# Performance work log

Measured on AMD Instinct MI355X. Metric: run time of the kernel, lower is better.

## Reference

```python
import jax, jax.numpy as jnp
import numpy as np

B, T, E = 1024, 200, 64
NU, NM, NC = 100000, 1000000, 1000
D_LAU_IN = 8 * E      # 512
D_MLP_IN = 7 * E      # 448
EPS = 1e-5
NEG = -2.0 ** 31


def setup_inputs() -> dict:
    key = jax.random.key(0)
    ks = jax.random.split(key, 32)
    f = lambda k, shape, s=0.05: (jax.random.normal(k, shape, dtype=jnp.float32) * s)
    inp = {
        "uid": jax.random.randint(ks[0], (B,), 0, NU, dtype=jnp.int32),
        "mid": jax.random.randint(ks[1], (B,), 0, NM, dtype=jnp.int32),
        "cat": jax.random.randint(ks[2], (B,), 0, NC, dtype=jnp.int32),
        "historical_mid": jax.random.randint(ks[3], (B, T), 0, NM, dtype=jnp.int32),
        "historical_cat": jax.random.randint(ks[4], (B, T), 0, NC, dtype=jnp.int32),
        "mask": jax.random.randint(ks[5], (B, T), 0, 2, dtype=jnp.int32),
        # embedding tables
        "user_table": f(ks[6], (NU, E), 0.1),
        "mat_table": f(ks[7], (NM, E), 0.1),
        "cat_table": f(ks[8], (NC, E), 0.1),
        # LocalActivationUnit: Linear(512,256)->Sigmoid->Linear(256,128)->Sigmoid->Linear(128,1)
        "lau_w1": f(ks[9], (D_LAU_IN, 256)), "lau_b1": f(ks[10], (256,)),
        "lau_w2": f(ks[11], (256, 128)),     "lau_b2": f(ks[12], (128,)),
        "lau_w3": f(ks[13], (128, 1)),       "lau_b3": f(ks[14], (1,)),
        # MLP: BN(448)->Linear(448,512)->BN->LeakyReLU(0.1)->Linear(512,256)->BN->LeakyReLU->Linear(256,2)
        "bn0_g": jnp.ones((D_MLP_IN,), jnp.float32), "bn0_b": jnp.zeros((D_MLP_IN,), jnp.float32),
        "mlp_w1": f(ks[15], (D_MLP_IN, 512)), "mlp_b1": f(ks[16], (512,)),
        "bn1_g": jnp.ones((512,), jnp.float32), "bn1_b": jnp.zeros((512,), jnp.float32),
        "mlp_w2": f(ks[17], (512, 256)),      "mlp_b2": f(ks[18], (256,)),
        "bn2_g": jnp.ones((256,), jnp.float32), "bn2_b": jnp.zeros((256,), jnp.float32),
        "mlp_w3": f(ks[19], (256, 2)),        "mlp_b3": f(ks[20], (2,)),
    }
    return inp


def _bn(x, g, b):
    # torch BatchNorm1d in training mode: batch mean, biased variance
    mu = jnp.mean(x, axis=0)
    var = jnp.var(x, axis=0)
    return (x - mu) * jax.lax.rsqrt(var + EPS) * g + b


def reference(uid, mid, cat, historical_mid, historical_cat, mask,
              user_table, mat_table, cat_table,
              lau_w1, lau_b1, lau_w2, lau_b2, lau_w3, lau_b3,
              bn0_g, bn0_b, mlp_w1, mlp_b1, bn1_g, bn1_b,
              mlp_w2, mlp_b2, bn2_g, bn2_b, mlp_w3, mlp_b3):
    u = user_table[uid]                                             # [B,E]
    cur = jnp.concatenate([mat_table[mid], cat_table[cat]], axis=1)  # [B,2E]
    hist = jnp.concatenate([mat_table[historical_mid],
                            cat_table[historical_cat]], axis=2)      # [B,T,2E]
    maskf = mask.astype(hist.dtype)                                  # [B,T]

    # Local activation unit
    cur_e = jnp.broadcast_to(cur[:, None, :], hist.shape)            # [B,T,2E]
    comb = jnp.concatenate([cur_e, hist, cur_e - hist, cur_e * hist], axis=2)  # [B,T,8E]
    h = jax.nn.sigmoid(comb @ lau_w1 + lau_b1)
    h = jax.nn.sigmoid(h @ lau_w2 + lau_b2)
    aw = (h @ lau_w3 + lau_b3)[..., 0]                               # [B,T]
    masked = jnp.where(mask == 1, aw, jnp.asarray(NEG, aw.dtype))
    scores = jax.nn.softmax(masked, axis=-1) * maskf                 # [B,T]
    lau = jnp.einsum('bt,bte->be', scores, hist)                     # [B,2E]

    # masked mean of history
    hsum = jnp.einsum('bt,bte->be', maskf, hist)
    hmean = hsum / jnp.sum(maskf, axis=1, keepdims=True)

    x = jnp.concatenate([u, cur, lau, hmean], axis=-1)               # [B,7E]
    x = _bn(x, bn0_g, bn0_b)
    x = jax.nn.leaky_relu(_bn(x @ mlp_w1 + mlp_b1, bn1_g, bn1_b), 0.1)
    x = jax.nn.leaky_relu(_bn(x @ mlp_w2 + mlp_b2, bn2_g, bn2_b), 0.1)
    return x @ mlp_w3 + mlp_b3                                        # [B,2]
```

## Files before the change

### kernel.cpp

```cpp
#include <hip/hip_runtime.h>

#define BB 1024
#define TT 200
#define MROWS (BB*TT)

typedef unsigned short u16;
typedef __attribute__((ext_vector_type(8))) short bf16x8;
typedef __attribute__((ext_vector_type(4))) float f32x4;

__device__ __forceinline__ u16 f2bf(float f) {
  unsigned u = __float_as_uint(f);
  u += 0x7fff + ((u >> 16) & 1);
  return (u16)(u >> 16);
}
__device__ __forceinline__ float bf2f(u16 h) {
  return __uint_as_float(((unsigned)h) << 16);
}

__global__ void prep_weights(const float* __restrict__ w1, const float* __restrict__ w2,
                             u16* __restrict__ WpT, float* __restrict__ Wq,
                             u16* __restrict__ W2T) {
  int i = blockIdx.x * 256 + threadIdx.x;
  if (i < 65536) {
    int n = i >> 8, k = i & 255;
    float v;
    if (k < 128) v = w1[(128 + k) * 256 + n] - w1[(256 + k) * 256 + n];
    else         v = w1[(384 + (k - 128)) * 256 + n];
    WpT[n * 256 + k] = f2bf(v);
  } else if (i < 98304) {
    int j = i - 65536;
    int k = j >> 8, jc = j & 255;
    Wq[j] = w1[k * 256 + jc] + w1[(256 + k) * 256 + jc];
  } else if (i < 131072) {
    int j = i - 98304;
    int n = j >> 8, k = j & 255;
    W2T[j] = f2bf(w2[k * 128 + n]);
  }
}

__global__ __launch_bounds__(256) void prep_batch(
    const int* __restrict__ mid, const int* __restrict__ cat,
    const float* __restrict__ mat_table, const float* __restrict__ cat_table,
    const float* __restrict__ lau_b1, const float* __restrict__ Wq,
    float* __restrict__ cur, float* __restrict__ bias1p) {
  int b = blockIdx.x, tid = threadIdx.x;
  __shared__ float curL[128];
  if (tid < 64)        curL[tid] = mat_table[(long)mid[b] * 64 + tid];
  else if (tid < 128)  curL[tid] = cat_table[(long)cat[b] * 64 + (tid - 64)];
  __syncthreads();
  if (tid < 128) cur[b * 128 + tid] = curL[tid];
  float s = lau_b1[tid];
  for (int k = 0; k < 128; ++k) s += curL[k] * Wq[k * 256 + tid];
  bias1p[b * 256 + tid] = s;
}

__global__ __launch_bounds__(256) void lau_fused(
    const int* __restrict__ hmid, const int* __restrict__ hcat,
    const float* __restrict__ mat_table, const float* __restrict__ cat_table,
    const float* __restrict__ cur, const float* __restrict__ bias1p,
    const u16* __restrict__ WpT, const u16* __restrict__ W2T,
    const float* __restrict__ b2, const float* __restrict__ w3,
    const float* __restrict__ b3,
    u16* __restrict__ Xh, float* __restrict__ AW) {
  __shared__ __align__(16) u16 Al[64 * 264];
  __shared__ float awp[4][64];
  int tid = threadIdx.x, wave = tid >> 6, l = tid & 63;
  int q = l >> 4, r16 = l & 15;
  long mBase = (long)blockIdx.x * 64;

  for (int i = tid; i < 2048; i += 256) {
    int r = i >> 5, c4 = i & 31;
    long bt = mBase + r;
    int b = (int)(bt / TT);
    int e0 = c4 * 4;
    float4 hv;
    if (e0 < 64) hv = *(const float4*)(mat_table + (long)hmid[bt] * 64 + e0);
    else         hv = *(const float4*)(cat_table + (long)hcat[bt] * 64 + (e0 - 64));
    float4 cv = *(const float4*)(cur + b * 128 + e0);
    u16 hb[4] = {f2bf(hv.x), f2bf(hv.y), f2bf(hv.z), f2bf(hv.w)};
    u16 pb[4] = {f2bf(hv.x * cv.x), f2bf(hv.y * cv.y), f2bf(hv.z * cv.z), f2bf(hv.w * cv.w)};
    *(ushort4*)(Al + r * 264 + e0)       = *(ushort4*)hb;
    *(ushort4*)(Al + r * 264 + 128 + e0) = *(ushort4*)pb;
    *(ushort4*)(Xh + bt * 128 + e0)      = *(ushort4*)hb;
  }
  __syncthreads();

  f32x4 acc1[4][4] = {};
  const u16* wp1 = WpT + ((long)(wave * 64 + r16)) * 256 + q * 8;
  #pragma unroll
  for (int ki = 0; ki < 8; ++ki) {
    bf16x8 a[4];
    #pragma unroll
    for (int mt = 0; mt < 4; ++mt)
      a[mt] = *(const bf16x8*)(Al + (mt * 16 + r16) * 264 + ki * 32 + q * 8);
    #pragma unroll
    for (int nt = 0; nt < 4; ++nt) {
      bf16x8 bq = *(const bf16x8*)(wp1 + nt * (16 * 256) + ki * 32);
      #pragma unroll
      for (int mt = 0; mt < 4; ++mt)
        acc1[mt][nt] = __builtin_amdgcn_mfma_f32_16x16x32_bf16(a[mt], bq, acc1[mt][nt], 0, 0, 0);
    }
  }
  __syncthreads();
  #pragma unroll
  for (int mt = 0; mt < 4; ++mt)
    #pragma unroll
    for (int r = 0; r < 4; ++r) {
      int row = mt * 16 + q * 4 + r;
      int bidx = (int)((mBase + row) / TT);
      const float* bp = bias1p + (long)bidx * 256;
      #pragma unroll
      for (int nt = 0; nt < 4; ++nt) {
        int col = wave * 64 + nt * 16 + r16;
        float z = acc1[mt][nt][r] + bp[col];
        Al[row * 264 + col] = f2bf(1.f / (1.f + __expf(-z)));
      }
    }
  __syncthreads();

  f32x4 acc2[4][2] = {};
  const u16* wp2 = W2T + ((long)(wave * 32 + r16)) * 256 + q * 8;
  #pragma unroll
  for (int ki = 0; ki < 8; ++ki) {
    bf16x8 a[4];
    #pragma unroll
    for (int mt = 0; mt < 4; ++mt)
      a[mt] = *(const bf16x8*)(Al + (mt * 16 + r16) * 264 + ki * 32 + q * 8);
    #pragma unroll
    for (int nt = 0; nt < 2; ++nt) {
      bf16x8 bq = *(const bf16x8*)(wp2 + nt * (16 * 256) + ki * 32);
      #pragma unroll
      for (int mt = 0; mt < 4; ++mt)
        acc2[mt][nt] = __builtin_amdgcn_mfma_f32_16x16x32_bf16(a[mt], bq, acc2[mt][nt], 0, 0, 0);
    }
  }
  float rp[4][4];
  #pragma unroll
  for (int mt = 0; mt < 4; ++mt)
    #pragma unroll
    for (int r = 0; r < 4; ++r) rp[mt][r] = 0.f;
  #pragma unroll
  for (int nt = 0; nt < 2; ++nt) {
    int col = wave * 32 + nt * 16 + r16;
    float b2v = b2[col], w3v = w3[col];
    #pragma unroll
    for (int mt = 0; mt < 4; ++mt)
      #pragma unroll
      for (int r = 0; r < 4; ++r) {
        float z = acc2[mt][nt][r] + b2v;
        rp[mt][r] += w3v / (1.f + __expf(-z));
      }
  }
  #pragma unroll
  for (int off = 1; off < 16; off <<= 1)
    #pragma unroll
    for (int mt = 0; mt < 4; ++mt)
      #pragma unroll
      for (int r = 0; r < 4; ++r)
        rp[mt][r] += __shfl_xor(rp[mt][r], off, 16);
  if (r16 == 0)
    #pragma unroll
    for (int mt = 0; mt < 4; ++mt)
      #pragma unroll
      for (int r = 0; r < 4; ++r)
        awp[wave][mt * 16 + q * 4 + r] = rp[mt][r];
  __syncthreads();
  if (tid < 64)
    AW[mBase + tid] = awp[0][tid] + awp[1][tid] + awp[2][tid] + awp[3][tid] + b3[0];
}

__global__ __launch_bounds__(256) void softmax_pool(
    const float* __restrict__ AW, const int* __restrict__ mask,
    const int* __restrict__ uid, const float* __restrict__ user_table,
    const float* __restrict__ cur, const u16* __restrict__ Xh,
    float* __restrict__ Xmlp) {
  int b = blockIdx.x, tid = threadIdx.x;
  __shared__ float red[256];
  __shared__ float sc[TT], mkf[TT];
  __shared__ float ps[512];
  int mk = 0;
  float masked = -3.0e38f;
  if (tid < TT) {
    mk = mask[b * TT + tid];
    masked = mk ? AW[b * TT + tid] : -2147483648.0f;
  }
  red[tid] = masked; __syncthreads();
  for (int s = 128; s > 0; s >>= 1) { if (tid < s) red[tid] = fmaxf(red[tid], red[tid + s]); __syncthreads(); }
  float mx = red[0]; __syncthreads();
  float ev = (tid < TT) ? __expf(masked - mx) : 0.f;
  red[tid] = ev; __syncthreads();
  for (int s = 128; s > 0; s >>= 1) { if (tid < s) red[tid] += red[tid + s]; __syncthreads(); }
  float denom = red[0]; __syncthreads();
  red[tid] = (tid < TT) ? (float)mk : 0.f; __syncthreads();
  for (int s = 128; s > 0; s >>= 1) { if (tid < s) red[tid] += red[tid + s]; __syncthreads(); }
  float cnt = red[0]; __syncthreads();
  if (tid < TT) { sc[tid] = (ev / denom) * (float)mk; mkf[tid] = (float)mk; }
  __syncthreads();
  int c = tid & 127, p = tid >> 7;
  const u16* xb = Xh + (long)b * TT * 128 + c;
  float sL = 0.f, sH = 0.f;
  for (int t = p; t < TT; t += 2) {
    float hv = bf2f(xb[(long)t * 128]);
    sL += sc[t] * hv;
    sH += mkf[t] * hv;
  }
  ps[tid] = sL; ps[256 + tid] = sH;
  __syncthreads();
  if (tid < 128) {
    float lau  = ps[tid] + ps[tid + 128];
    float hsum = ps[256 + tid] + ps[256 + tid + 128];
    Xmlp[b * 448 + 192 + tid] = lau;
    Xmlp[b * 448 + 320 + tid] = hsum / cnt;
  } else {
    int j = tid - 128;
    Xmlp[b * 448 + 64 + j] = cur[b * 128 + j];
    if (j < 64) Xmlp[b * 448 + j] = user_table[(long)uid[b] * 64 + j];
  }
}

__global__ __launch_bounds__(256) void colstats(const float* __restrict__ X, int cols,
                                                float* __restrict__ psum,
                                                float* __restrict__ psq) {
  int cg = blockIdx.x, rc = blockIdx.y;
  int c = threadIdx.x & 63, ty = threadIdx.x >> 6;
  int col = cg * 64 + c;
  float s = 0.f, ss = 0.f;
  for (int i = 0; i < 16; ++i) {
    int r = rc * 64 + ty + i * 4;
    float v = X[(long)r * cols + col];
    s += v; ss += v * v;
  }
  __shared__ float s1[256], s2[256];
  s1[threadIdx.x] = s; s2[threadIdx.x] = ss;
  __syncthreads();
  if (ty == 0) {
    s  = s1[c] + s1[c + 64] + s1[c + 128] + s1[c + 192];
    ss = s2[c] + s2[c + 64] + s2[c + 128] + s2[c + 192];
    psum[rc * cols + col] = s;
    psq [rc * cols + col] = ss;
  }
}

template <bool LEAKY>
__global__ __launch_bounds__(256) void gemm_bn(
    const float* __restrict__ A, int K,
    const float* __restrict__ psumA, const float* __restrict__ psqA,
    const float* __restrict__ g, const float* __restrict__ bta,
    const float* __restrict__ W, const float* __restrict__ bias, int N,
    float* __restrict__ C, float* __restrict__ psumC, float* __restrict__ psqC) {
  __shared__ float As[16][65], Bs[16][65];
  __shared__ float scK[512], shK[512];
  __shared__ float colS[16][64], colQ[16][64];
  int tid = threadIdx.x;
  for (int j = tid; j < K; j += 256) {
    float s = 0.f, ss = 0.f;
    for (int rc = 0; rc < 16; ++rc) { s += psumA[rc * K + j]; ss += psqA[rc * K + j]; }
    float mu = s * (1.f / 1024.f), var = ss * (1.f / 1024.f) - mu * mu;
    float scv = rsqrtf(var + 1e-5f) * g[j];
    scK[j] = scv; shK[j] = bta[j] - mu * scv;
  }
  __syncthreads();
  int m0 = blockIdx.x * 64, n0 = blockIdx.y * 64;
  int tx = tid & 15, ty = tid >> 4;
  float acc[4][4] = {};
  for (int k0 = 0; k0 < K; k0 += 16) {
    __syncthreads();
    for (int i = tid; i < 1024; i += 256) {
      int m = i >> 4, k = i & 15;
      float v = A[(long)(m0 + m) * K + k0 + k] * scK[k0 + k] + shK[k0 + k];
      if (LEAKY) v = v > 0.f ? v : 0.1f * v;
      As[k][m] = v;
    }
    for (int i = tid; i < 1024; i += 256) {
      int k = i >> 6, n = i & 63;
      Bs[k][n] = W[(long)(k0 + k) * N + n0 + n];
    }
    __syncthreads();
    for (int k = 0; k < 16; ++k) {
      float a[4], bq[4];
      for (int ii = 0; ii < 4; ++ii) a[ii]  = As[k][ty * 4 + ii];
      for (int jj = 0; jj < 4; ++jj) bq[jj] = Bs[k][tx * 4 + jj];
      for (int ii = 0; ii < 4; ++ii)
        for (int jj = 0; jj < 4; ++jj) acc[ii][jj] += a[ii] * bq[jj];
    }
  }
  float cs4[4], cq4[4];
  for (int jj = 0; jj < 4; ++jj) {
    int n = n0 + tx * 4 + jj;
    float bv = bias[n];
    float cs = 0.f, cq = 0.f;
    for (int ii = 0; ii < 4; ++ii) {
      float val = acc[ii][jj] + bv;
      C[(long)(m0 + ty * 4 + ii) * N + n] = val;
      cs += val; cq += val * val;
    }
    cs4[jj] = cs; cq4[jj] = cq;
  }
  __syncthreads();
  for (int jj = 0; jj < 4; ++jj) {
    colS[ty][tx * 4 + jj] = cs4[jj];
    colQ[ty][tx * 4 + jj] = cq4[jj];
  }
  __syncthreads();
  if (tid < 64) {
    float s = 0.f, ss = 0.f;
    for (int t = 0; t < 16; ++t) { s += colS[t][tid]; ss += colQ[t][tid]; }
    psumC[blockIdx.x * N + n0 + tid] = s;
    psqC [blockIdx.x * N + n0 + tid] = ss;
  }
}

__global__ __launch_bounds__(256) void final_out(
    const float* __restrict__ y2,
    const float* __restrict__ psum2, const float* __restrict__ psq2,
    const float* __restrict__ g, const float* __restrict__ bta,
    const float* __restrict__ w3, const float* __restrict__ b3,
    float* __restrict__ out) {
  __shared__ float sc2[256], sh2[256];
  __shared__ float p0[256], p1[256];
  int tid = threadIdx.x;
  {
    float s = 0.f, ss = 0.f;
    for (int rc = 0; rc < 16; ++rc) { s += psum2[rc * 256 + tid]; ss += psq2[rc * 256 + tid]; }
    float mu = s * (1.f / 1024.f), var = ss * (1.f / 1024.f) - mu * mu;
    float scv = rsqrtf(var + 1e-5f) * g[tid];
    sc2[tid] = scv; sh2[tid] = bta[tid] - mu * scv;
  }
  __syncthreads();
  int row = blockIdx.x * 64 + (tid >> 2), q = tid & 3;
  const float* yr = y2 + (long)row * 256;
  float a0 = 0.f, a1 = 0.f;
  for (int k = q * 64; k < q * 64 + 64; ++k) {
    float v = yr[k] * sc2[k] + sh2[k];
    v = v > 0.f ? v : 0.1f * v;
    a0 += v * w3[2 * k];
    a1 += v * w3[2 * k + 1];
  }
  p0[tid] = a0; p1[tid] = a1;
  __syncthreads();
  if (q == 0) {
    out[row * 2 + 0] = p0[tid] + p0[tid + 1] + p0[tid + 2] + p0[tid + 3] + b3[0];
    out[row * 2 + 1] = p1[tid] + p1[tid + 1] + p1[tid + 2] + p1[tid + 3] + b3[1];
  }
}


extern "C" void kernel_launch(void* const* d_in, const int* in_sizes, int n_in,
                              void* d_out, int out_size, void* d_ws, size_t ws_size,
                              hipStream_t stream) {
  const int* uid  = (const int*)d_in[0];
  const int* mid  = (const int*)d_in[1];
  const int* cat  = (const int*)d_in[2];
  const int* hmid = (const int*)d_in[3];
  const int* hcat = (const int*)d_in[4];
  const int* mask = (const int*)d_in[5];
  const float* user_table = (const float*)d_in[6];
  const float* mat_table  = (const float*)d_in[7];
  const float* cat_table  = (const float*)d_in[8];
  const float* lau_w1 = (const float*)d_in[9];
  const float* lau_b1 = (const float*)d_in[10];
  const float* lau_w2 = (const float*)d_in[11];
  const float* lau_b2 = (const float*)d_in[12];
  const float* lau_w3 = (const float*)d_in[13];
  const float* lau_b3 = (const float*)d_in[14];
  const float* bn0_g = (const float*)d_in[15];
  const float* bn0_b = (const float*)d_in[16];
  const float* mlp_w1 = (const float*)d_in[17];
  const float* mlp_b1 = (const float*)d_in[18];
  const float* bn1_g = (const float*)d_in[19];
  const float* bn1_b = (const float*)d_in[20];
  const float* mlp_w2 = (const float*)d_in[21];
  const float* mlp_b2 = (const float*)d_in[22];
  const float* bn2_g = (const float*)d_in[23];
  const float* bn2_b = (const float*)d_in[24];
  const float* mlp_w3 = (const float*)d_in[25];
  const float* mlp_b3 = (const float*)d_in[26];
  float* out = (float*)d_out;

  char* w = (char*)d_ws;
  size_t off = 0;
  auto take = [&](size_t bytes) { size_t o = off; off += (bytes + 255) & ~(size_t)255; return o; };
  u16*   Xh     = (u16*)  (w + take((size_t)MROWS * 128 * 2));
  float* AW     = (float*)(w + take((size_t)MROWS * 4));
  float* cur    = (float*)(w + take((size_t)BB * 128 * 4));
  float* bias1p = (float*)(w + take((size_t)BB * 256 * 4));
  float* xmlp   = (float*)(w + take((size_t)BB * 448 * 4));
  float* y1     = (float*)(w + take((size_t)BB * 512 * 4));
  float* y2     = (float*)(w + take((size_t)BB * 256 * 4));
  u16*   WpT    = (u16*)  (w + take(256 * 256 * 2));
  float* Wq     = (float*)(w + take(128 * 256 * 4));
  u16*   W2T    = (u16*)  (w + take(128 * 256 * 2));
  float* psum0  = (float*)(w + take(16 * 448 * 4));
  float* psq0   = (float*)(w + take(16 * 448 * 4));
  float* psum1  = (float*)(w + take(16 * 512 * 4));
  float* psq1   = (float*)(w + take(16 * 512 * 4));
  float* psum2  = (float*)(w + take(16 * 256 * 4));
  float* psq2   = (float*)(w + take(16 * 256 * 4));

  prep_weights<<<512, 256, 0, stream>>>(lau_w1, lau_w2, WpT, Wq, W2T);
  prep_batch<<<BB, 256, 0, stream>>>(mid, cat, mat_table, cat_table, lau_b1, Wq, cur, bias1p);
  lau_fused<<<MROWS / 64, 256, 0, stream>>>(hmid, hcat, mat_table, cat_table, cur, bias1p,
                                            WpT, W2T, lau_b2, lau_w3, lau_b3, Xh, AW);
  softmax_pool<<<BB, 256, 0, stream>>>(AW, mask, uid, user_table, cur, Xh, xmlp);
  {
    dim3 g(448 / 64, 16);
    colstats<<<g, 256, 0, stream>>>(xmlp, 448, psum0, psq0);
  }
  {
    dim3 g(16, 512 / 64);
    gemm_bn<false><<<g, 256, 0, stream>>>(xmlp, 448, psum0, psq0, bn0_g, bn0_b,
                                          mlp_w1, mlp_b1, 512, y1, psum1, psq1);
  }
  {
    dim3 g(16, 256 / 64);
    gemm_bn<true><<<g, 256, 0, stream>>>(y1, 512, psum1, psq1, bn1_g, bn1_b,
                                         mlp_w2, mlp_b2, 256, y2, psum2, psq2);
  }
  final_out<<<16, 256, 0, stream>>>(y2, psum2, psq2, bn2_g, bn2_b, mlp_w3, mlp_b3, out);
}
```

Before: 748.1 us.

## Fuse attention MLP, softmax and pooling into one per-batch kernel

Replaces the row-tiled LAU kernel and separate softmax/pool kernel with a single kernel per batch row (448 threads) that gathers all 200 history embeddings into LDS, runs layer1→sigmoid→layer2 chained per 32-column chunk through a small per-wave scratch, then does masked softmax and pooling from LDS. This removes the global round-trip of the bf16 history buffer and attention weights and one launch. It also computes the history×current products on the fly from LDS and uses rcp-based sigmoid. Risk: weights are re-read from global per chunk per wave, only 1024 blocks, and padding rows (200→224) add wasted MFMA work.

```diff
diff --git a/kernel.cpp b/kernel.cpp
--- a/kernel.cpp
+++ b/kernel.cpp
@@ -2,7 +2,9 @@
 
 #define BB 1024
 #define TT 200
-#define MROWS (BB*TT)
+#define TP 224
+#define BT 448
+#define NEGF (-2147483648.0f)
 
 typedef unsigned short u16;
 typedef __attribute__((ext_vector_type(8))) short bf16x8;
@@ -15,6 +17,9 @@
 }
 __device__ __forceinline__ float bf2f(u16 h) {
   return __uint_as_float(((unsigned)h) << 16);
+}
+__device__ __forceinline__ float fast_sigmoid(float z) {
+  return __builtin_amdgcn_rcpf(1.f + __expf(-z));
 }
 
 __global__ void prep_weights(const float* __restrict__ w1, const float* __restrict__ w2,
@@ -42,179 +47,188 @@
     const int* __restrict__ mid, const int* __restrict__ cat,
     const float* __restrict__ mat_table, const float* __restrict__ cat_table,
     const float* __restrict__ lau_b1, const float* __restrict__ Wq,
-    float* __restrict__ cur, float* __restrict__ bias1p) {
+    float* __restrict__ bias1p) {
   int b = blockIdx.x, tid = threadIdx.x;
   __shared__ float curL[128];
   if (tid < 64)        curL[tid] = mat_table[(long)mid[b] * 64 + tid];
   else if (tid < 128)  curL[tid] = cat_table[(long)cat[b] * 64 + (tid - 64)];
   __syncthreads();
-  if (tid < 128) cur[b * 128 + tid] = curL[tid];
   float s = lau_b1[tid];
   for (int k = 0; k < 128; ++k) s += curL[k] * Wq[k * 256 + tid];
   bias1p[b * 256 + tid] = s;
 }
 
-__global__ __launch_bounds__(256) void lau_fused(
+__global__ __launch_bounds__(BT, 4) void din_fused(
+    const int* __restrict__ uid, const int* __restrict__ mid,
+    const int* __restrict__ cat,
     const int* __restrict__ hmid, const int* __restrict__ hcat,
+    const int* __restrict__ mask,
+    const float* __restrict__ user_table,
     const float* __restrict__ mat_table, const float* __restrict__ cat_table,
-    const float* __restrict__ cur, const float* __restrict__ bias1p,
+    const float* __restrict__ bias1p,
     const u16* __restrict__ WpT, const u16* __restrict__ W2T,
     const float* __restrict__ b2, const float* __restrict__ w3,
     const float* __restrict__ b3,
-    u16* __restrict__ Xh, float* __restrict__ AW) {
-  __shared__ __align__(16) u16 Al[64 * 264];
-  __shared__ float awp[4][64];
+    float* __restrict__ xmlp) {
+  __shared__ __align__(16) u16 histL[TP][136];
+  __shared__ __align__(16) u16 scratch[7][16][40];
+  __shared__ __align__(16) float curL[128];
+  __shared__ float biasL[256];
+  __shared__ float b2L[128], w3L[128];
+  __shared__ float awL[TP];
+
   int tid = threadIdx.x, wave = tid >> 6, l = tid & 63;
   int q = l >> 4, r16 = l & 15;
-  long mBase = (long)blockIdx.x * 64;
-
-  for (int i = tid; i < 2048; i += 256) {
-    int r = i >> 5, c4 = i & 31;
-    long bt = mBase + r;
-    int b = (int)(bt / TT);
-    int e0 = c4 * 4;
+  int b = blockIdx.x;
+
+  if (tid < 256) biasL[tid] = bias1p[b * 256 + tid];
+  if (tid >= 256 && tid < 384) { b2L[tid - 256] = b2[tid - 256]; w3L[tid - 256] = w3[tid - 256]; }
+  if (tid >= 384 && tid < 448) curL[tid - 384] = mat_table[(long)mid[b] * 64 + (tid - 384)];
+  if (tid < 64)                curL[64 + tid]  = cat_table[(long)cat[b] * 64 + tid];
+  float b3v = b3[0];
+  for (int j = tid; j < 1632; j += BT)
+    ((unsigned*)&histL[200][0])[j] = 0;
+
+  const int* hm = hmid + b * TT;
+  const int* hc = hcat + b * TT;
+  #pragma unroll 4
+  for (int i = tid; i < 6400; i += BT) {
+    int r = i >> 5, c4 = i & 31, e0 = c4 * 4;
     float4 hv;
-    if (e0 < 64) hv = *(const float4*)(mat_table + (long)hmid[bt] * 64 + e0);
-    else         hv = *(const float4*)(cat_table + (long)hcat[bt] * 64 + (e0 - 64));
-    float4 cv = *(const float4*)(cur + b * 128 + e0);
+    if (e0 < 64) hv = *(const float4*)(mat_table + (long)hm[r] * 64 + e0);
+    else         hv = *(const float4*)(cat_table + (long)hc[r] * 64 + (e0 - 64));
     u16 hb[4] = {f2bf(hv.x), f2bf(hv.y), f2bf(hv.z), f2bf(hv.w)};
-    u16 pb[4] = {f2bf(hv.x * cv.x), f2bf(hv.y * cv.y), f2bf(hv.z * cv.z), f2bf(hv.w * cv.w)};
-    *(ushort4*)(Al + r * 264 + e0)       = *(ushort4*)hb;
-    *(ushort4*)(Al + r * 264 + 128 + e0) = *(ushort4*)pb;
-    *(ushort4*)(Xh + bt * 128 + e0)      = *(ushort4*)hb;
-  }
-  __syncthreads();
-
-  f32x4 acc1[4][4] = {};
-  const u16* wp1 = WpT + ((long)(wave * 64 + r16)) * 256 + q * 8;
-  #pragma unroll
-  for (int ki = 0; ki < 8; ++ki) {
-    bf16x8 a[4];
+    *(ushort4*)(&histL[r][e0]) = *(ushort4*)hb;
+  }
+  __syncthreads();
+
+  for (int mt = 0; mt < 2; ++mt) {
+    int tile = wave * 2 + mt;
+    bf16x8 afr[8];
     #pragma unroll
-    for (int mt = 0; mt < 4; ++mt)
-      a[mt] = *(const bf16x8*)(Al + (mt * 16 + r16) * 264 + ki * 32 + q * 8);
+    for (int k4 = 0; k4 < 4; ++k4) {
+      bf16x8 h = *(const bf16x8*)(&histL[tile * 16 + r16][k4 * 32 + q * 8]);
+      afr[k4] = h;
+      float4 c0 = *(const float4*)(&curL[k4 * 32 + q * 8]);
+      float4 c1 = *(const float4*)(&curL[k4 * 32 + q * 8 + 4]);
+      bf16x8 pr;
+      pr[0] = (short)f2bf(bf2f((u16)h[0]) * c0.x);
+      pr[1] = (short)f2bf(bf2f((u16)h[1]) * c0.y);
+      pr[2] = (short)f2bf(bf2f((u16)h[2]) * c0.z);
+      pr[3] = (short)f2bf(bf2f((u16)h[3]) * c0.w);
+      pr[4] = (short)f2bf(bf2f((u16)h[4]) * c1.x);
+      pr[5] = (short)f2bf(bf2f((u16)h[5]) * c1.y);
+      pr[6] = (short)f2bf(bf2f((u16)h[6]) * c1.z);
+      pr[7] = (short)f2bf(bf2f((u16)h[7]) * c1.w);
+      afr[4 + k4] = pr;
+    }
+
+    f32x4 acc2[8] = {};
+    for (int nc = 0; nc < 8; ++nc) {
+      f32x4 acc1[2] = {};
+      const u16* wpb = WpT + (nc * 32 + r16) * 256 + q * 8;
+      bf16x8 bf0 = *(const bf16x8*)(wpb);
+      bf16x8 bf1 = *(const bf16x8*)(wpb + 4096);
+      #pragma unroll
+      for (int ki = 0; ki < 8; ++ki) {
+        bf16x8 b0 = bf0, b1 = bf1;
+        if (ki < 7) {
+          bf0 = *(const bf16x8*)(wpb + (ki + 1) * 32);
+          bf1 = *(const bf16x8*)(wpb + 4096 + (ki + 1) * 32);
+        }
+        acc1[0] = __builtin_amdgcn_mfma_f32_16x16x32_bf16(afr[ki], b0, acc1[0], 0, 0, 0);
+        acc1[1] = __builtin_amdgcn_mfma_f32_16x16x32_bf16(afr[ki], b1, acc1[1], 0, 0, 0);
+      }
+      #pragma unroll
+      for (int bn = 0; bn < 2; ++bn)
+        #pragma unroll
+        for (int r = 0; r < 4; ++r) {
+          float z = acc1[bn][r] + biasL[nc * 32 + bn * 16 + r16];
+          scratch[wave][q * 4 + r][bn * 16 + r16] = f2bf(fast_sigmoid(z));
+        }
+      __builtin_amdgcn_wave_barrier();
+      bf16x8 a2 = *(const bf16x8*)(&scratch[wave][r16][q * 8]);
+      __builtin_amdgcn_wave_barrier();
+      const u16* w2b = W2T + r16 * 256 + nc * 32 + q * 8;
+      #pragma unroll
+      for (int n2 = 0; n2 < 8; ++n2)
+        acc2[n2] = __builtin_amdgcn_mfma_f32_16x16x32_bf16(
+            a2, *(const bf16x8*)(w2b + n2 * 4096), acc2[n2], 0, 0, 0);
+    }
+    float rp[4] = {0.f, 0.f, 0.f, 0.f};
     #pragma unroll
-    for (int nt = 0; nt < 4; ++nt) {
-      bf16x8 bq = *(const bf16x8*)(wp1 + nt * (16 * 256) + ki * 32);
-      #pragma unroll
-      for (int mt = 0; mt < 4; ++mt)
-        acc1[mt][nt] = __builtin_amdgcn_mfma_f32_16x16x32_bf16(a[mt], bq, acc1[mt][nt], 0, 0, 0);
-    }
-  }
-  __syncthreads();
-  #pragma unroll
-  for (int mt = 0; mt < 4; ++mt)
+    for (int n2 = 0; n2 < 8; ++n2) {
+      float b2v = b2L[n2 * 16 + r16], w3v = w3L[n2 * 16 + r16];
+      #pragma unroll
+      for (int r = 0; r < 4; ++r)
+        rp[r] += w3v * fast_sigmoid(acc2[n2][r] + b2v);
+    }
     #pragma unroll
-    for (int r = 0; r < 4; ++r) {
-      int row = mt * 16 + q * 4 + r;
-      int bidx = (int)((mBase + row) / TT);
-      const float* bp = bias1p + (long)bidx * 256;
-      #pragma unroll
-      for (int nt = 0; nt < 4; ++nt) {
-        int col = wave * 64 + nt * 16 + r16;
-        float z = acc1[mt][nt][r] + bp[col];
-        Al[row * 264 + col] = f2bf(1.f / (1.f + __expf(-z)));
-      }
-    }
-  __syncthreads();
-
-  f32x4 acc2[4][2] = {};
-  const u16* wp2 = W2T + ((long)(wave * 32 + r16)) * 256 + q * 8;
-  #pragma unroll
-  for (int ki = 0; ki < 8; ++ki) {
-    bf16x8 a[4];
-    #pragma unroll
-    for (int mt = 0; mt < 4; ++mt)
-      a[mt] = *(const bf16x8*)(Al + (mt * 16 + r16) * 264 + ki * 32 + q * 8);
-    #pragma unroll
-    for (int nt = 0; nt < 2; ++nt) {
-      bf16x8 bq = *(const bf16x8*)(wp2 + nt * (16 * 256) + ki * 32);
-      #pragma unroll
-      for (int mt = 0; mt < 4; ++mt)
-        acc2[mt][nt] = __builtin_amdgcn_mfma_f32_16x16x32_bf16(a[mt], bq, acc2[mt][nt], 0, 0, 0);
-    }
-  }
-  float rp[4][4];
-  #pragma unroll
-  for (int mt = 0; mt < 4; ++mt)
-    #pragma unroll
-    for (int r = 0; r < 4; ++r) rp[mt][r] = 0.f;
-  #pragma unroll
-  for (int nt = 0; nt < 2; ++nt) {
-    int col = wave * 32 + nt * 16 + r16;
-    float b2v = b2[col], w3v = w3[col];
-    #pragma unroll
-    for (int mt = 0; mt < 4; ++mt)
-      #pragma unroll
-      for (int r = 0; r < 4; ++r) {
-        float z = acc2[mt][nt][r] + b2v;
-        rp[mt][r] += w3v / (1.f + __expf(-z));
-      }
-  }
-  #pragma unroll
-  for (int off = 1; off < 16; off <<= 1)
-    #pragma unroll
-    for (int mt = 0; mt < 4; ++mt)
+    for (int off = 1; off < 16; off <<= 1)
       #pragma unroll
       for (int r = 0; r < 4; ++r)
-        rp[mt][r] += __shfl_xor(rp[mt][r], off, 16);
-  if (r16 == 0)
-    #pragma unroll
-    for (int mt = 0; mt < 4; ++mt)
+        rp[r] += __shfl_xor(rp[r], off, 16);
+    if (r16 == 0)
       #pragma unroll
       for (int r = 0; r < 4; ++r)
-        awp[wave][mt * 16 + q * 4 + r] = rp[mt][r];
-  __syncthreads();
-  if (tid < 64)
-    AW[mBase + tid] = awp[0][tid] + awp[1][tid] + awp[2][tid] + awp[3][tid] + b3[0];
-}
-
-__global__ __launch_bounds__(256) void softmax_pool(
-    const float* __restrict__ AW, const int* __restrict__ mask,
-    const int* __restrict__ uid, const float* __restrict__ user_table,
-    const float* __restrict__ cur, const u16* __restrict__ Xh,
-    float* __restrict__ Xmlp) {
-  int b = blockIdx.x, tid = threadIdx.x;
-  __shared__ float red[256];
-  __shared__ float sc[TT], mkf[TT];
-  __shared__ float ps[512];
-  int mk = 0;
-  float masked = -3.0e38f;
-  if (tid < TT) {
-    mk = mask[b * TT + tid];
-    masked = mk ? AW[b * TT + tid] : -2147483648.0f;
-  }
-  red[tid] = masked; __syncthreads();
-  for (int s = 128; s > 0; s >>= 1) { if (tid < s) red[tid] = fmaxf(red[tid], red[tid + s]); __syncthreads(); }
-  float mx = red[0]; __syncthreads();
+        awL[tile * 16 + q * 4 + r] = rp[r] + b3v;
+  }
+  __syncthreads();
+
+  float* scL   = (float*)&scratch[0][0][0];
+  float* mkL   = scL + 224;
+  float* redA  = scL + 448;
+  float* redB  = scL + 704;
+  float* poolL = scL + 960;
+  float* poolH = scL + 1344;
+
+  int mk = 0; float masked = NEGF;
+  if (tid < TT) { mk = mask[b * TT + tid]; masked = mk ? awL[tid] : NEGF; }
+  if (tid < 256) redA[tid] = masked;
+  __syncthreads();
+  for (int s = 128; s > 0; s >>= 1) {
+    if (tid < s) redA[tid] = fmaxf(redA[tid], redA[tid + s]);
+    __syncthreads();
+  }
+  float mx = redA[0];
+  __syncthreads();
   float ev = (tid < TT) ? __expf(masked - mx) : 0.f;
-  red[tid] = ev; __syncthreads();
-  for (int s = 128; s > 0; s >>= 1) { if (tid < s) red[tid] += red[tid + s]; __syncthreads(); }
-  float denom = red[0]; __syncthreads();
-  red[tid] = (tid < TT) ? (float)mk : 0.f; __syncthreads();
-  for (int s = 128; s > 0; s >>= 1) { if (tid < s) red[tid] += red[tid + s]; __syncthreads(); }
-  float cnt = red[0]; __syncthreads();
-  if (tid < TT) { sc[tid] = (ev / denom) * (float)mk; mkf[tid] = (float)mk; }
-  __syncthreads();
-  int c = tid & 127, p = tid >> 7;
-  const u16* xb = Xh + (long)b * TT * 128 + c;
-  float sL = 0.f, sH = 0.f;
-  for (int t = p; t < TT; t += 2) {
-    float hv = bf2f(xb[(long)t * 128]);
-    sL += sc[t] * hv;
-    sH += mkf[t] * hv;
-  }
-  ps[tid] = sL; ps[256 + tid] = sH;
-  __syncthreads();
-  if (tid < 128) {
-    float lau  = ps[tid] + ps[tid + 128];
-    float hsum = ps[256 + tid] + ps[256 + tid + 128];
-    Xmlp[b * 448 + 192 + tid] = lau;
-    Xmlp[b * 448 + 320 + tid] = hsum / cnt;
+  if (tid < 256) { redA[tid] = ev; redB[tid] = (tid < TT) ? (float)mk : 0.f; }
+  __syncthreads();
+  for (int s = 128; s > 0; s >>= 1) {
+    if (tid < s) { redA[tid] += redA[tid + s]; redB[tid] += redB[tid + s]; }
+    __syncthreads();
+  }
+  float rden = __builtin_amdgcn_rcpf(redA[0]);
+  float cnt  = redB[0];
+  __syncthreads();
+  if (tid < TT) { scL[tid] = ev * rden * (float)mk; mkL[tid] = (float)mk; }
+  __syncthreads();
+
+  if (tid < 384) {
+    int c = tid & 127, p = tid >> 7;
+    float sL = 0.f, sH = 0.f;
+    for (int t = p; t < TT; t += 3) {
+      float hv = bf2f(histL[t][c]);
+      sL += scL[t] * hv;
+      sH += mkL[t] * hv;
+    }
+    poolL[p * 128 + c] = sL;
+    poolH[p * 128 + c] = sH;
+  }
+  __syncthreads();
+
+  float rcnt = __builtin_amdgcn_rcpf(cnt);
+  if (tid < 64) {
+    xmlp[b * 448 + tid] = user_table[(long)uid[b] * 64 + tid];
+  } else if (tid < 192) {
+    xmlp[b * 448 + tid] = curL[tid - 64];
+  } else if (tid < 320) {
+    int c = tid - 192;
+    xmlp[b * 448 + tid] = poolL[c] + poolL[128 + c] + poolL[256 + c];
   } else {
-    int j = tid - 128;
-    Xmlp[b * 448 + 64 + j] = cur[b * 128 + j];
-    if (j < 64) Xmlp[b * 448 + j] = user_table[(long)uid[b] * 64 + j];
+    int c = tid - 320;
+    xmlp[b * 448 + tid] = (poolH[c] + poolH[128 + c] + poolH[256 + c]) * rcnt;
   }
 }
 
@@ -327,10 +341,10 @@
     sc2[tid] = scv; sh2[tid] = bta[tid] - mu * scv;
   }
   __syncthreads();
-  int row = blockIdx.x * 64 + (tid >> 2), q = tid & 3;
+  int row = blockIdx.x * 64 + (tid >> 2), qq = tid & 3;
   const float* yr = y2 + (long)row * 256;
   float a0 = 0.f, a1 = 0.f;
-  for (int k = q * 64; k < q * 64 + 64; ++k) {
+  for (int k = qq * 64; k < qq * 64 + 64; ++k) {
     float v = yr[k] * sc2[k] + sh2[k];
     v = v > 0.f ? v : 0.1f * v;
     a0 += v * w3[2 * k];
@@ -338,7 +352,7 @@
   }
   p0[tid] = a0; p1[tid] = a1;
   __syncthreads();
-  if (q == 0) {
+  if (qq == 0) {
     out[row * 2 + 0] = p0[tid] + p0[tid + 1] + p0[tid + 2] + p0[tid + 3] + b3[0];
     out[row * 2 + 1] = p1[tid] + p1[tid + 1] + p1[tid + 2] + p1[tid + 3] + b3[1];
   }
@@ -380,9 +394,6 @@
   char* w = (char*)d_ws;
   size_t off = 0;
   auto take = [&](size_t bytes) { size_t o = off; off += (bytes + 255) & ~(size_t)255; return o; };
-  u16*   Xh     = (u16*)  (w + take((size_t)MROWS * 128 * 2));
-  float* AW     = (float*)(w + take((size_t)MROWS * 4));
-  float* cur    = (float*)(w + take((size_t)BB * 128 * 4));
   float* bias1p = (float*)(w + take((size_t)BB * 256 * 4));
   float* xmlp   = (float*)(w + take((size_t)BB * 448 * 4));
   float* y1     = (float*)(w + take((size_t)BB * 512 * 4));
@@ -398,10 +409,10 @@
   float* psq2   = (float*)(w + take(16 * 256 * 4));
 
   prep_weights<<<512, 256, 0, stream>>>(lau_w1, lau_w2, WpT, Wq, W2T);
-  prep_batch<<<BB, 256, 0, stream>>>(mid, cat, mat_table, cat_table, lau_b1, Wq, cur, bias1p);
-  lau_fused<<<MROWS / 64, 256, 0, stream>>>(hmid, hcat, mat_table, cat_table, cur, bias1p,
-                                            WpT, W2T, lau_b2, lau_w3, lau_b3, Xh, AW);
-  softmax_pool<<<BB, 256, 0, stream>>>(AW, mask, uid, user_table, cur, Xh, xmlp);
+  prep_batch<<<BB, 256, 0, stream>>>(mid, cat, mat_table, cat_table, lau_b1, Wq, bias1p);
+  din_fused<<<BB, BT, 0, stream>>>(uid, mid, cat, hmid, hcat, mask,
+                                   user_table, mat_table, cat_table,
+                                   bias1p, WpT, W2T, lau_b2, lau_w3, lau_b3, xmlp);
   {
     dim3 g(448 / 64, 16);
     colstats<<<g, 256, 0, stream>>>(xmlp, 448, psum0, psq0);
```

Measured after the change: 903.2 us. +20.7%, slower.
